# Optimization experiments

Hardware: AMD Instinct MI355X
Metric: run time of the kernel (lower is better)

The kernel has to match this reference:

```python
import jax, jax.numpy as jnp
import numpy as np

B, T, D, H, L = 8192, 80, 32, 64, 3


def setup_inputs() -> dict:
    key = jax.random.key(0)
    ks = jax.random.split(key, 16)
    s = lambda k, shape, fan: jax.random.normal(k, shape, jnp.float32) / np.sqrt(fan)
    inp = {"x": jax.random.normal(ks[0], (B, T, D), jnp.float32)}
    dims_in = [D, H, H]
    i = 1
    for l in range(L):
        din = dims_in[l]
        inp[f"W_ih{l}"] = s(ks[i], (H, din), H); i += 1
        inp[f"W_hh{l}"] = s(ks[i], (H, H), H); i += 1
        inp[f"b_ih{l}"] = s(ks[i], (H,), H); i += 1
        inp[f"b_hh{l}"] = s(ks[i], (H,), H); i += 1
    inp["W_fc"] = s(ks[i], (1, H), H); i += 1
    inp["b_fc"] = s(ks[i], (1,), H)
    return inp


def _rnn_layer(xs, W_ih, W_hh, b_ih, b_hh):
    # xs: [T, B, Din] -> ys: [T, B, H]; tanh RNN recurrence (PyTorch nn.RNN math)
    pre = jnp.einsum('tbd,hd->tbh', xs, W_ih) + b_ih + b_hh  # input proj precomputed
    h0 = jnp.zeros((xs.shape[1], W_hh.shape[0]), xs.dtype)
    def step(h, p):
        h_new = jnp.tanh(p + h @ W_hh.T)
        return h_new, h_new
    _, ys = jax.lax.scan(step, h0, pre)
    return ys


def reference(x, W_ih0, W_hh0, b_ih0, b_hh0, W_ih1, W_hh1, b_ih1, b_hh1,
              W_ih2, W_hh2, b_ih2, b_hh2, W_fc, b_fc):
    # x: [B, T, D] (batch_first) -> time-major [T, B, D]
    h = jnp.swapaxes(x, 0, 1)
    params = [(W_ih0, W_hh0, b_ih0, b_hh0),
              (W_ih1, W_hh1, b_ih1, b_hh1),
              (W_ih2, W_hh2, b_ih2, b_hh2)]
    for (W_ih, W_hh, b_ih, b_hh) in params:
        h = _rnn_layer(h, W_ih, W_hh, b_ih, b_hh)
    last = h[-1]                      # [B, H] == out[:, -1, :]
    return last @ W_fc.T + b_fc       # [B, 1]
```

## Files before the change

kernel.cpp:

```cpp
#include <hip/hip_runtime.h>
#include <hip/hip_bf16.h>
#include <cstddef>


typedef __attribute__((ext_vector_type(8))) short s16x8;
typedef __attribute__((ext_vector_type(4))) short s16x4;
typedef __attribute__((ext_vector_type(4))) float fx4;

#define MFMA16(A, B, C) __builtin_amdgcn_mfma_f32_16x16x32_bf16((A), (B), (C), 0, 0, 0)

#if __has_builtin(__builtin_amdgcn_exp2f)
#define EXP2F(x) __builtin_amdgcn_exp2f(x)
#else
#define EXP2F(x) exp2f(x)
#endif
#if __has_builtin(__builtin_amdgcn_rcpf)
#define RCPF(x) __builtin_amdgcn_rcpf(x)
#else
#define RCPF(x) (1.0f / (x))
#endif

static constexpr float K2LOG2E = 2.8853900817779268f;

__device__ __forceinline__ short f2bf(float f) {
  union { float f; unsigned u; } v; v.f = f;
  unsigned r = v.u + 0x7FFFu + ((v.u >> 16) & 1u);
  return (short)(r >> 16);
}
__device__ __forceinline__ float bf2f(short s) {
  union { unsigned u; float f; } v; v.u = ((unsigned)(unsigned short)s) << 16;
  return v.f;
}
__device__ __forceinline__ unsigned pk2bf(float a, float b) {
  float2 t; t.x = a; t.y = b;
  union { __hip_bfloat162 h; unsigned u; } c;
  c.h = __float22bfloat162_rn(t);
  return c.u;
}

__device__ __forceinline__ s16x8 wfragA(const float* W, int ncols, int row, int col0) {
  const float* p = W + row * ncols + col0;
  s16x8 r;
#pragma unroll
  for (int i = 0; i < 8; ++i) r[i] = f2bf(p[i]);
  return r;
}

__device__ __forceinline__ void act_store(fx4 acc, const float* bsc, short* wp) {
  float h[4];
#pragma unroll
  for (int r = 0; r < 4; ++r) {
    float e = EXP2F(__builtin_fmaf(acc[r], K2LOG2E, bsc[r]));
    h[r] = 1.f - 2.f * RCPF(e + 1.f);
  }
  union { unsigned u[2]; s16x4 v; } p;
  p.u[0] = pk2bf(h[0], h[1]);
  p.u[1] = pk2bf(h[2], h[3]);
  *(s16x4*)wp = p.v;
}

__global__ __launch_bounds__(256, 2) void rnn3_mfma4(
    const float* __restrict__ x,
    const float* __restrict__ Wih0, const float* __restrict__ Whh0,
    const float* __restrict__ bih0, const float* __restrict__ bhh0,
    const float* __restrict__ Wih1, const float* __restrict__ Whh1,
    const float* __restrict__ bih1, const float* __restrict__ bhh1,
    const float* __restrict__ Wih2, const float* __restrict__ Whh2,
    const float* __restrict__ bih2, const float* __restrict__ bhh2,
    const float* __restrict__ Wfc, const float* __restrict__ bfc,
    float* __restrict__ out)
{
  __shared__ __align__(16) short hb[3][16][72];

  const int tid = threadIdx.x;
  const int wv  = tid >> 6;
  const int ln  = tid & 63;
  const int q   = ln >> 4;
  const int m15 = ln & 15;
  const int bbase = (int)blockIdx.x * 16;

  const int arow = 16 * wv + m15;
  s16x8 wih0 = wfragA(Wih0, 32, arow, 8 * q);
  s16x8 whh0[2], wih1[2], whh1[2], wih2[2], whh2[2];
#pragma unroll
  for (int kf = 0; kf < 2; ++kf) {
    const int c = 32 * kf + 8 * q;
    whh0[kf] = wfragA(Whh0, 64, arow, c);
    wih1[kf] = wfragA(Wih1, 64, arow, c);
    whh1[kf] = wfragA(Whh1, 64, arow, c);
    wih2[kf] = wfragA(Wih2, 64, arow, c);
    whh2[kf] = wfragA(Whh2, 64, arow, c);
  }

  float b0[4], b1[4], b2[4];
#pragma unroll
  for (int r = 0; r < 4; ++r) {
    const int j = 16 * wv + 4 * q + r;
    b0[r] = (bih0[j] + bhh0[j]) * K2LOG2E;
    b1[r] = (bih1[j] + bhh1[j]) * K2LOG2E;
    b2[r] = (bih2[j] + bhh2[j]) * K2LOG2E;
  }

  const fx4 z4 = {0.f, 0.f, 0.f, 0.f};
  const s16x8 z8 = {0, 0, 0, 0, 0, 0, 0, 0};
  s16x8 rec0a = z8, rec0b = z8, rec1a = z8, rec1b = z8, rec2a = z8, rec2b = z8;

  short* wr0 = &hb[0][m15][16 * wv + 4 * q];
  short* wr1 = &hb[1][m15][16 * wv + 4 * q];
  short* wr2 = &hb[2][m15][16 * wv + 4 * q];
  const short* rd0 = &hb[0][m15][8 * q];
  const short* rd1 = &hb[1][m15][8 * q];
  const short* rd2 = &hb[2][m15][8 * q];

  const float* xr = x + (size_t)(bbase + m15) * (80 * 32) + 8 * q;
  fx4 xc0 = *(const fx4*)(xr);
  fx4 xc1 = *(const fx4*)(xr + 4);

  for (int t = 0; t < 80; ++t) {
    union { unsigned u[4]; s16x8 v; } xp;
    xp.u[0] = pk2bf(xc0[0], xc0[1]); xp.u[1] = pk2bf(xc0[2], xc0[3]);
    xp.u[2] = pk2bf(xc1[0], xc1[1]); xp.u[3] = pk2bf(xc1[2], xc1[3]);

    fx4 aA = MFMA16(wih0, xp.v, z4);
    fx4 aB = MFMA16(whh0[0], rec0a, z4);
    aB = MFMA16(whh0[1], rec0b, aB);
    act_store(aA + aB, b0, wr0);
    __syncthreads();

    const int tn = (t < 79) ? t + 1 : 79;
    fx4 xn0 = *(const fx4*)(xr + tn * 32);
    fx4 xn1 = *(const fx4*)(xr + tn * 32 + 4);

    s16x8 in0 = *(const s16x8*)(rd0);
    s16x8 in1 = *(const s16x8*)(rd0 + 32);
    aA = MFMA16(whh1[0], rec1a, z4);
    aA = MFMA16(whh1[1], rec1b, aA);
    aB = MFMA16(wih1[0], in0, z4);
    aB = MFMA16(wih1[1], in1, aB);
    act_store(aA + aB, b1, wr1);
    __syncthreads();
    rec0a = in0; rec0b = in1;

    s16x8 j0 = *(const s16x8*)(rd1);
    s16x8 j1 = *(const s16x8*)(rd1 + 32);
    aA = MFMA16(whh2[0], rec2a, z4);
    aA = MFMA16(whh2[1], rec2b, aA);
    aB = MFMA16(wih2[0], j0, z4);
    aB = MFMA16(wih2[1], j1, aB);
    act_store(aA + aB, b2, wr2);
    __syncthreads();
    rec1a = j0; rec1b = j1;
    rec2a = *(const s16x8*)(rd2);
    rec2b = *(const s16x8*)(rd2 + 32);

    xc0 = xn0; xc1 = xn1;
  }

  float s = 0.f;
#pragma unroll
  for (int i = 0; i < 8; ++i) s += bf2f(rec2a[i]) * Wfc[8 * q + i];
#pragma unroll
  for (int i = 0; i < 8; ++i) s += bf2f(rec2b[i]) * Wfc[32 + 8 * q + i];
  s += __shfl_xor(s, 16, 64);
  s += __shfl_xor(s, 32, 64);
  if (wv == 0 && ln < 16) out[bbase + ln] = s + bfc[0];
}

extern "C" void kernel_launch(void* const* d_in, const int* in_sizes, int n_in,
                              void* d_out, int out_size, void* d_ws, size_t ws_size,
                              hipStream_t stream) {
  const float* x    = (const float*)d_in[0];
  const float* Wih0 = (const float*)d_in[1];
  const float* Whh0 = (const float*)d_in[2];
  const float* bih0 = (const float*)d_in[3];
  const float* bhh0 = (const float*)d_in[4];
  const float* Wih1 = (const float*)d_in[5];
  const float* Whh1 = (const float*)d_in[6];
  const float* bih1 = (const float*)d_in[7];
  const float* bhh1 = (const float*)d_in[8];
  const float* Wih2 = (const float*)d_in[9];
  const float* Whh2 = (const float*)d_in[10];
  const float* bih2 = (const float*)d_in[11];
  const float* bhh2 = (const float*)d_in[12];
  const float* Wfc  = (const float*)d_in[13];
  const float* bfc  = (const float*)d_in[14];

  rnn3_mfma4<<<dim3(512), dim3(256), 0, stream>>>(
      x, Wih0, Whh0, bih0, bhh0, Wih1, Whh1, bih1, bhh1,
      Wih2, Whh2, bih2, bhh2, Wfc, bfc, (float*)d_out);
}
```

Before: 202.8 us.

## Assign one wave per RNN layer and pipeline layers as a wavefront

Result: faster. 196.2 us (-3.3%).

```diff
diff --git a/kernel.cpp b/kernel.cpp
--- a/kernel.cpp
+++ b/kernel.cpp
@@ -27,10 +27,6 @@
   unsigned r = v.u + 0x7FFFu + ((v.u >> 16) & 1u);
   return (short)(r >> 16);
 }
-__device__ __forceinline__ float bf2f(short s) {
-  union { unsigned u; float f; } v; v.u = ((unsigned)(unsigned short)s) << 16;
-  return v.f;
-}
 __device__ __forceinline__ unsigned pk2bf(float a, float b) {
   float2 t; t.x = a; t.y = b;
   union { __hip_bfloat162 h; unsigned u; } c;
@@ -46,20 +42,7 @@
   return r;
 }
 
-__device__ __forceinline__ void act_store(fx4 acc, const float* bsc, short* wp) {
-  float h[4];
-#pragma unroll
-  for (int r = 0; r < 4; ++r) {
-    float e = EXP2F(__builtin_fmaf(acc[r], K2LOG2E, bsc[r]));
-    h[r] = 1.f - 2.f * RCPF(e + 1.f);
-  }
-  union { unsigned u[2]; s16x4 v; } p;
-  p.u[0] = pk2bf(h[0], h[1]);
-  p.u[1] = pk2bf(h[2], h[3]);
-  *(s16x4*)wp = p.v;
-}
-
-__global__ __launch_bounds__(256, 2) void rnn3_mfma4(
+__global__ __launch_bounds__(192, 2) void rnn3_pipe(
     const float* __restrict__ x,
     const float* __restrict__ Wih0, const float* __restrict__ Whh0,
     const float* __restrict__ bih0, const float* __restrict__ bhh0,
@@ -70,7 +53,7 @@
     const float* __restrict__ Wfc, const float* __restrict__ bfc,
     float* __restrict__ out)
 {
-  __shared__ __align__(16) short hb[3][16][72];
+  __shared__ __align__(16) short hb[3][2][16][72];
 
   const int tid = threadIdx.x;
   const int wv  = tid >> 6;
@@ -79,91 +62,103 @@
   const int m15 = ln & 15;
   const int bbase = (int)blockIdx.x * 16;
 
-  const int arow = 16 * wv + m15;
-  s16x8 wih0 = wfragA(Wih0, 32, arow, 8 * q);
-  s16x8 whh0[2], wih1[2], whh1[2], wih2[2], whh2[2];
+  const float* Wih = (wv == 0) ? Wih0 : (wv == 1) ? Wih1 : Wih2;
+  const float* Whh = (wv == 0) ? Whh0 : (wv == 1) ? Whh1 : Whh2;
+  const float* bi  = (wv == 0) ? bih0 : (wv == 1) ? bih1 : bih2;
+  const float* bh  = (wv == 0) ? bhh0 : (wv == 1) ? bhh1 : bhh2;
+  const int kin = (wv == 0) ? 32 : 64;
+
+  s16x8 wi0[4], wi1[4], wh0[4], wh1[4];
+  const s16x8 z8 = {0, 0, 0, 0, 0, 0, 0, 0};
 #pragma unroll
-  for (int kf = 0; kf < 2; ++kf) {
-    const int c = 32 * kf + 8 * q;
-    whh0[kf] = wfragA(Whh0, 64, arow, c);
-    wih1[kf] = wfragA(Wih1, 64, arow, c);
-    whh1[kf] = wfragA(Whh1, 64, arow, c);
-    wih2[kf] = wfragA(Wih2, 64, arow, c);
-    whh2[kf] = wfragA(Whh2, 64, arow, c);
+  for (int tile = 0; tile < 4; ++tile) {
+    const int row = 16 * tile + m15;
+    wi0[tile] = wfragA(Wih, kin, row, 8 * q);
+    wi1[tile] = wv ? wfragA(Wih, 64, row, 32 + 8 * q) : z8;
+    wh0[tile] = wfragA(Whh, 64, row, 8 * q);
+    wh1[tile] = wfragA(Whh, 64, row, 32 + 8 * q);
   }
 
-  float b0[4], b1[4], b2[4];
+  float bsc[4][4];
 #pragma unroll
-  for (int r = 0; r < 4; ++r) {
-    const int j = 16 * wv + 4 * q + r;
-    b0[r] = (bih0[j] + bhh0[j]) * K2LOG2E;
-    b1[r] = (bih1[j] + bhh1[j]) * K2LOG2E;
-    b2[r] = (bih2[j] + bhh2[j]) * K2LOG2E;
+  for (int tile = 0; tile < 4; ++tile)
+#pragma unroll
+    for (int r = 0; r < 4; ++r) {
+      const int j = 16 * tile + 4 * q + r;
+      bsc[tile][r] = (bi[j] + bh[j]) * K2LOG2E;
+    }
+
+  const fx4 z4 = {0.f, 0.f, 0.f, 0.f};
+  s16x8 r0 = z8, r1 = z8;
+
+  const float* xr = x + (size_t)(bbase + m15) * (80 * 32) + 8 * q;
+  fx4 xc0 = {0,0,0,0}, xc1 = {0,0,0,0};
+  if (wv == 0) { xc0 = *(const fx4*)(xr); xc1 = *(const fx4*)(xr + 4); }
+
+  float hk[4][4];
+
+  for (int tau = 0; tau < 82; ++tau) {
+    const int lt = tau - wv;
+    if (0 <= lt && lt < 80) {
+      const int p = lt & 1;
+      s16x8 in0, in1;
+      if (wv) {
+        const short* up = &hb[wv - 1][p][m15][8 * q];
+        in0 = *(const s16x8*)(up);
+        in1 = *(const s16x8*)(up + 32);
+      } else {
+        union { unsigned u[4]; s16x8 v; } xp;
+        xp.u[0] = pk2bf(xc0[0], xc0[1]); xp.u[1] = pk2bf(xc0[2], xc0[3]);
+        xp.u[2] = pk2bf(xc1[0], xc1[1]); xp.u[3] = pk2bf(xc1[2], xc1[3]);
+        in0 = xp.v; in1 = z8;
+        const int tn = (lt < 79) ? lt + 1 : 79;
+        xc0 = *(const fx4*)(xr + tn * 32);
+        xc1 = *(const fx4*)(xr + tn * 32 + 4);
+      }
+      fx4 acc[4];
+#pragma unroll
+      for (int tile = 0; tile < 4; ++tile) acc[tile] = MFMA16(wh0[tile], r0, z4);
+#pragma unroll
+      for (int tile = 0; tile < 4; ++tile) acc[tile] = MFMA16(wh1[tile], r1, acc[tile]);
+#pragma unroll
+      for (int tile = 0; tile < 4; ++tile) acc[tile] = MFMA16(wi0[tile], in0, acc[tile]);
+      if (wv) {
+#pragma unroll
+        for (int tile = 0; tile < 4; ++tile) acc[tile] = MFMA16(wi1[tile], in1, acc[tile]);
+      }
+      short* wb = &hb[wv][p][m15][4 * q];
+#pragma unroll
+      for (int tile = 0; tile < 4; ++tile) {
+        float h[4];
+#pragma unroll
+        for (int r = 0; r < 4; ++r) {
+          float e = EXP2F(__builtin_fmaf(acc[tile][r], K2LOG2E, bsc[tile][r]));
+          h[r] = __builtin_fmaf(-2.f, RCPF(e + 1.f), 1.f);
+          hk[tile][r] = h[r];
+        }
+        union { unsigned u[2]; s16x4 v; } pk;
+        pk.u[0] = pk2bf(h[0], h[1]);
+        pk.u[1] = pk2bf(h[2], h[3]);
+        *(s16x4*)(wb + 16 * tile) = pk.v;
+      }
+      const short* ow = &hb[wv][p][m15][8 * q];
+      r0 = *(const s16x8*)(ow);
+      r1 = *(const s16x8*)(ow + 32);
+    }
+    __syncthreads();
   }
 
-  const fx4 z4 = {0.f, 0.f, 0.f, 0.f};
-  const s16x8 z8 = {0, 0, 0, 0, 0, 0, 0, 0};
-  s16x8 rec0a = z8, rec0b = z8, rec1a = z8, rec1b = z8, rec2a = z8, rec2b = z8;
-
-  short* wr0 = &hb[0][m15][16 * wv + 4 * q];
-  short* wr1 = &hb[1][m15][16 * wv + 4 * q];
-  short* wr2 = &hb[2][m15][16 * wv + 4 * q];
-  const short* rd0 = &hb[0][m15][8 * q];
-  const short* rd1 = &hb[1][m15][8 * q];
-  const short* rd2 = &hb[2][m15][8 * q];
-
-  const float* xr = x + (size_t)(bbase + m15) * (80 * 32) + 8 * q;
-  fx4 xc0 = *(const fx4*)(xr);
-  fx4 xc1 = *(const fx4*)(xr + 4);
-
-  for (int t = 0; t < 80; ++t) {
-    union { unsigned u[4]; s16x8 v; } xp;
-    xp.u[0] = pk2bf(xc0[0], xc0[1]); xp.u[1] = pk2bf(xc0[2], xc0[3]);
-    xp.u[2] = pk2bf(xc1[0], xc1[1]); xp.u[3] = pk2bf(xc1[2], xc1[3]);
-
-    fx4 aA = MFMA16(wih0, xp.v, z4);
-    fx4 aB = MFMA16(whh0[0], rec0a, z4);
-    aB = MFMA16(whh0[1], rec0b, aB);
-    act_store(aA + aB, b0, wr0);
-    __syncthreads();
-
-    const int tn = (t < 79) ? t + 1 : 79;
-    fx4 xn0 = *(const fx4*)(xr + tn * 32);
-    fx4 xn1 = *(const fx4*)(xr + tn * 32 + 4);
-
-    s16x8 in0 = *(const s16x8*)(rd0);
-    s16x8 in1 = *(const s16x8*)(rd0 + 32);
-    aA = MFMA16(whh1[0], rec1a, z4);
-    aA = MFMA16(whh1[1], rec1b, aA);
-    aB = MFMA16(wih1[0], in0, z4);
-    aB = MFMA16(wih1[1], in1, aB);
-    act_store(aA + aB, b1, wr1);
-    __syncthreads();
-    rec0a = in0; rec0b = in1;
-
-    s16x8 j0 = *(const s16x8*)(rd1);
-    s16x8 j1 = *(const s16x8*)(rd1 + 32);
-    aA = MFMA16(whh2[0], rec2a, z4);
-    aA = MFMA16(whh2[1], rec2b, aA);
-    aB = MFMA16(wih2[0], j0, z4);
-    aB = MFMA16(wih2[1], j1, aB);
-    act_store(aA + aB, b2, wr2);
-    __syncthreads();
-    rec1a = j0; rec1b = j1;
-    rec2a = *(const s16x8*)(rd2);
-    rec2b = *(const s16x8*)(rd2 + 32);
-
-    xc0 = xn0; xc1 = xn1;
+  if (wv == 2) {
+    float s = 0.f;
+#pragma unroll
+    for (int tile = 0; tile < 4; ++tile)
+#pragma unroll
+      for (int r = 0; r < 4; ++r)
+        s += hk[tile][r] * Wfc[16 * tile + 4 * q + r];
+    s += __shfl_xor(s, 16, 64);
+    s += __shfl_xor(s, 32, 64);
+    if (ln < 16) out[bbase + ln] = s + bfc[0];
   }
-
-  float s = 0.f;
-#pragma unroll
-  for (int i = 0; i < 8; ++i) s += bf2f(rec2a[i]) * Wfc[8 * q + i];
-#pragma unroll
-  for (int i = 0; i < 8; ++i) s += bf2f(rec2b[i]) * Wfc[32 + 8 * q + i];
-  s += __shfl_xor(s, 16, 64);
-  s += __shfl_xor(s, 32, 64);
-  if (wv == 0 && ln < 16) out[bbase + ln] = s + bfc[0];
 }
 
 extern "C" void kernel_launch(void* const* d_in, const int* in_sizes, int n_in,
@@ -185,7 +180,7 @@
   const float* Wfc  = (const float*)d_in[13];
   const float* bfc  = (const float*)d_in[14];
 
-  rnn3_mfma4<<<dim3(512), dim3(256), 0, stream>>>(
+  rnn3_pipe<<<dim3(512), dim3(192), 0, stream>>>(
       x, Wih0, Whh0, bih0, bhh0, Wih1, Whh1, bih1, bhh1,
       Wih2, Whh2, bih2, bhh2, Wfc, bfc, (float*)d_out);
 }
```
